# Optimization experiments

Hardware: AMD Instinct MI355X
Metric: run time of the kernel (lower is better)

The kernel has to match this reference:

```python
import jax, jax.numpy as jnp
import numpy as np

IN_SIZE = 512
HID = 512
BATCH = 65536


def setup_inputs() -> dict:
    key = jax.random.key(0)
    ks = jax.random.split(key, 20)
    s = 1.0 / np.sqrt(IN_SIZE)
    sh = 1.0 / np.sqrt(HID)
    d = {
        "inputs": jax.random.normal(ks[0], (BATCH, IN_SIZE), jnp.float32),
        "state": jax.random.normal(ks[1], (BATCH, HID), jnp.float32),
        "parent_state": jax.random.normal(ks[2], (BATCH, HID), jnp.float32),
    }
    # input-path linears (with bias), torch Linear layout: W [out, in], y = x @ W.T + b
    for i, name in enumerate(["w_a", "w_r", "w_r1", "w_c"]):
        d[name + "_w"] = jax.random.uniform(ks[3 + 2 * i], (HID, IN_SIZE), jnp.float32, -s, s)
        d[name + "_b"] = jax.random.uniform(ks[4 + 2 * i], (HID,), jnp.float32, -s, s)
    # state-path and parent-path linears (no bias)
    for i, name in enumerate(["u_a", "u_r", "u_r1", "u_c", "p_a", "p_r", "p_r1", "p_c"]):
        d[name + "_w"] = jax.random.uniform(ks[11 + i], (HID, HID), jnp.float32, -sh, sh)
    return d


def reference(inputs, state, parent_state,
              w_a_w, w_a_b, w_r_w, w_r_b, w_r1_w, w_r1_b, w_c_w, w_c_b,
              u_a_w, u_r_w, u_r1_w, u_c_w,
              p_a_w, p_r_w, p_r1_w, p_c_w):
    def lin(x, w, b=None):
        y = x @ w.T
        return y if b is None else y + b

    att = jax.nn.sigmoid(lin(inputs, w_a_w, w_a_b) + lin(state, u_a_w) + lin(parent_state, p_a_w))
    r = jax.nn.sigmoid(lin(inputs, w_r_w, w_r_b) + lin(state, u_r_w) + lin(parent_state, p_r_w))
    r1 = jax.nn.sigmoid(lin(inputs, w_r1_w, w_r1_b) + lin(state, u_r1_w) + lin(parent_state, p_r1_w))
    c = jnp.tanh(lin(inputs, w_c_w, w_c_b) + lin(state * r, u_c_w) + lin(parent_state * r1, p_c_w))
    new_h = att * c + (1.0 - att) * state
    return new_h
```

## Files before the change

### kernel.cpp

```cpp
#include <hip/hip_runtime.h>
#include <stdint.h>


typedef unsigned short u16;
using bf16x8 = __attribute__((ext_vector_type(8))) __bf16;
using f32x4  = __attribute__((ext_vector_type(4))) float;

__device__ __forceinline__ u16 f2bf(float f) {
    __bf16 b = (__bf16)f;
    union { __bf16 b; u16 u; } v; v.b = b;
    return v.u;
}
__device__ __forceinline__ uint32_t f2bf2(float lo, float hi) {
    return (uint32_t)f2bf(lo) | ((uint32_t)f2bf(hi) << 16);
}
__device__ __forceinline__ float bf2f(u16 s) {
    union { uint32_t u; float f; } v; v.u = ((uint32_t)s) << 16;
    return v.f;
}
__device__ __forceinline__ void load_lds16(const void* g, void* l) {
    __builtin_amdgcn_global_load_lds(
        (const __attribute__((address_space(1))) uint32_t*)g,
        (__attribute__((address_space(3))) uint32_t*)l, 16, 0, 0);
}
__device__ __forceinline__ void fence_bar() {
    asm volatile("" ::: "memory");
    __builtin_amdgcn_s_barrier();
    asm volatile("" ::: "memory");
}

__global__ void prep_weights(
    const float* __restrict__ wa, const float* __restrict__ ua, const float* __restrict__ pa,
    const float* __restrict__ wrg, const float* __restrict__ ur, const float* __restrict__ pr,
    const float* __restrict__ wr1, const float* __restrict__ ur1, const float* __restrict__ pr1,
    const float* __restrict__ wcc, const float* __restrict__ uc, const float* __restrict__ pc,
    u16* __restrict__ B1, u16* __restrict__ B2)
{
    int idx = blockIdx.x * 256 + threadIdx.x;
    const int T1 = 1536 * 1536;
    if (idx < T1) {
        int n = idx / 1536, k = idx - n * 1536;
        int g = n >> 9, nn = n & 511;
        int o = k >> 9, kk = k & 511;
        const float* s;
        if (g == 0)      s = (o == 0) ? wa  : (o == 1) ? ua  : pa;
        else if (g == 1) s = (o == 0) ? wrg : (o == 1) ? ur  : pr;
        else             s = (o == 0) ? wr1 : (o == 1) ? ur1 : pr1;
        B1[idx] = f2bf(s[nn * 512 + kk]);
    } else {
        int j = idx - T1;
        if (j < 512 * 1536) {
            int n = j / 1536, k = j - n * 1536;
            int o = k >> 9, kk = k & 511;
            const float* s = (o == 0) ? wcc : (o == 1) ? uc : pc;
            B2[j] = f2bf(s[n * 512 + kk]);
        }
    }
}

__global__ void cast_inputs(const float* __restrict__ X, const float* __restrict__ H,
                            const float* __restrict__ P,
                            u16* __restrict__ Xb, u16* __restrict__ Hb, u16* __restrict__ Pb)
{
    const long long MAT8 = (65536LL * 512) / 8;
    for (long long t = (long long)blockIdx.x * 256 + threadIdx.x;
         t < 3 * MAT8; t += (long long)gridDim.x * 256) {
        int m = (int)(t >> 22);
        long long e = (t & (MAT8 - 1)) * 8;
        const float* s = (m == 0) ? X : (m == 1) ? H : P;
        u16* d = (m == 0) ? Xb : (m == 1) ? Hb : Pb;
        f32x4 a = *(const f32x4*)(s + e);
        f32x4 b = *(const f32x4*)(s + e + 4);
        uint4 q;
        q.x = f2bf2(a.x, a.y); q.y = f2bf2(a.z, a.w);
        q.z = f2bf2(b.x, b.y); q.w = f2bf2(b.z, b.w);
        *(uint4*)(d + e) = q;
    }
}

template<int MODE>
__global__ __launch_bounds__(512, 2)
void gemm256(const u16* __restrict__ A0, const u16* __restrict__ A1s, const u16* __restrict__ A2s,
             const u16* __restrict__ Bw,
             const float* __restrict__ bias0, const float* __restrict__ bias1,
             const float* __restrict__ bias2,
             const u16* __restrict__ HbP, const u16* __restrict__ PbP,
             const float* __restrict__ Hf,
             float* __restrict__ outp, u16* __restrict__ hrw, u16* __restrict__ pr1w)
{
    __shared__ u16 lds[65536];
    constexpr int NT = 24;

    const int tid  = threadIdx.x;
    const int lane = tid & 63;
    const int wv   = tid >> 6;
    const int wr   = wv >> 2;
    const int wc   = wv & 3;

    int panel, ntl;
    const int xcd = blockIdx.x & 7;
    const int idx = blockIdx.x >> 3;
    if (MODE == 1) { panel = xcd * 32 + idx / 6;    ntl = idx % 6; }
    else           { panel = xcd * 32 + (idx >> 1); ntl = idx & 1; }
    const int m0 = panel * 256;
    const int n0 = ntl * 256;

    const int srow = tid >> 3;
    const int scg  = ((tid & 7) ^ (srow & 7)) * 8;
    const int ldst = srow * 64 + (tid & 7) * 8;

    const int ofsA = srow * 512 + scg;
    const int ofsB = srow * 1536 + scg;
    const u16* const bA0 = A0  + (size_t)m0 * 512;
    const u16* const bA1 = A1s + (size_t)m0 * 512;
    const u16* const bA2 = A2s + (size_t)m0 * 512;
    const u16* const bB  = Bw  + (size_t)n0 * 1536;
    u16* const ldA = lds + ldst;
    u16* const ldB = lds + 16384 + ldst;

    const int fr = lane & 15;
    const int fk = (lane >> 4) * 8;
    const int sw = (lane & 7) * 8;
    const int c0 = fk ^ sw;
    const int c1 = (32 + fk) ^ sw;
    const int aOff = (wr * 128 + fr) * 64;
    const int bOff = 16384 + (wc * 64 + fr) * 64;

    f32x4 acc[8][4];
    const f32x4 vzero = {0.0f, 0.0f, 0.0f, 0.0f};
#pragma unroll
    for (int i = 0; i < 8; ++i)
#pragma unroll
        for (int j = 0; j < 4; ++j) acc[i][j] = vzero;

    auto stA = [&](const u16* sA, int buf, int h) {
        const u16* g = sA + ofsA + h * 65536;
        u16* l = ldA + buf * 32768 + h * 8192;
        load_lds16(g, l);
        load_lds16(g + 64 * 512, l + 4096);
    };
    auto stB = [&](int T, int h) {
        const u16* g = bB + T * 64 + ofsB + h * 196608;
        u16* l = ldB + (T & 1) * 32768 + h * 8192;
        load_lds16(g, l);
        load_lds16(g + 64 * 1536, l + 4096);
    };

    stA(bA0, 0, 0); stA(bA0, 0, 1);
    stB(0, 0); stB(0, 1);
    stB(1, 0); stB(1, 1);
    asm volatile("s_waitcnt vmcnt(4)" ::: "memory");
    fence_bar();

    for (int T = 0; T < NT; ++T) {
        const int cb = (T & 1) * 32768;
        const int Tn = T + 1;
        const u16* sAn = ((Tn < 8) ? bA0 : (Tn < 16) ? bA1 : bA2) + (Tn & 7) * 64;
        const u16* const pa0 = lds + (cb + aOff + c0);
        const u16* const pa1 = lds + (cb + aOff + c1);
        const u16* const pb0 = lds + (cb + bOff + c0);
        const u16* const pb1 = lds + (cb + bOff + c1);

        bf16x8 bF[4][2];
#pragma unroll
        for (int q = 0; q < 4; ++q) {
            if (q == 0) {
#pragma unroll
                for (int j = 0; j < 4; ++j) {
                    bF[j][0] = *(const bf16x8*)(pb0 + j * 1024);
                    bF[j][1] = *(const bf16x8*)(pb1 + j * 1024);
                }
            }
            bf16x8 aF[2][2];
#pragma unroll
            for (int i = 0; i < 2; ++i) {
                aF[i][0] = *(const bf16x8*)(pa0 + (q * 2 + i) * 1024);
                aF[i][1] = *(const bf16x8*)(pa1 + (q * 2 + i) * 1024);
            }

            if (q == 0) { if (T < NT - 1) stA(sAn, Tn & 1, 0); }
            if (q == 1) { if (T < NT - 1) stA(sAn, Tn & 1, 1);
                          if (T < NT - 2) stB(T + 2, 0); }
            if (q == 2) { if (T < NT - 2) stB(T + 2, 1); }

            fence_bar();
            asm volatile("s_waitcnt lgkmcnt(0)" ::: "memory");
            __builtin_amdgcn_sched_barrier(0);
            __builtin_amdgcn_s_setprio(1);
#pragma unroll
            for (int i = 0; i < 2; ++i)
#pragma unroll
                for (int j = 0; j < 4; ++j)
#pragma unroll
                    for (int ks = 0; ks < 2; ++ks)
                        acc[q * 2 + i][j] = __builtin_amdgcn_mfma_f32_16x16x32_bf16(
                            aF[i][ks], bF[j][ks], acc[q * 2 + i][j], 0, 0, 0);
            __builtin_amdgcn_s_setprio(0);
            if (q == 3) {
                if (T < NT - 2)       asm volatile("s_waitcnt vmcnt(4)" ::: "memory");
                else if (T == NT - 2) asm volatile("s_waitcnt vmcnt(0)" ::: "memory");
            }
            fence_bar();
        }
    }

    const int rbase = m0 + wr * 128 + (lane >> 4) * 4;
    if (MODE == 1) {
        const int g = ntl >> 1;
        const float* bias = (g == 0) ? bias0 : (g == 1) ? bias1 : bias2;
        const int ncb = (ntl & 1) * 256 + wc * 64;
#pragma unroll
        for (int i = 0; i < 8; ++i)
#pragma unroll
            for (int j = 0; j < 4; ++j) {
                const int nn = ncb + j * 16 + fr;
                const float b = bias[nn];
                int off = (rbase + i * 16) * 512 + nn;
#pragma unroll
                for (int jj = 0; jj < 4; ++jj, off += 512) {
                    float v = acc[i][j][jj] + b;
                    float s = 1.0f / (1.0f + __expf(-v));
                    if (g == 0)      outp[off] = s;
                    else if (g == 1) hrw[off]  = f2bf(s * bf2f(HbP[off]));
                    else             pr1w[off] = f2bf(s * bf2f(PbP[off]));
                }
            }
    } else {
        const int ncb = n0 + wc * 64;
#pragma unroll
        for (int i = 0; i < 8; ++i)
#pragma unroll
            for (int j = 0; j < 4; ++j) {
                const int nn = ncb + j * 16 + fr;
                const float b = bias0[nn];
                int off = (rbase + i * 16) * 512 + nn;
#pragma unroll
                for (int jj = 0; jj < 4; ++jj, off += 512) {
                    float v = acc[i][j][jj] + b;
                    float e = __expf(2.0f * v);
                    float ct = 1.0f - 2.0f / (e + 1.0f);
                    float a = outp[off];
                    outp[off] = a * ct + (1.0f - a) * Hf[off];
                }
            }
    }
}

__global__ __launch_bounds__(256, 2)
void k1_small(const float* __restrict__ X, const float* __restrict__ H,
              const float* __restrict__ P, const u16* __restrict__ B1,
              const float* __restrict__ ba, const float* __restrict__ br,
              const float* __restrict__ br1,
              float* __restrict__ attf, u16* __restrict__ hrw, u16* __restrict__ pr1w)
{
    __shared__ u16 Ab[2][128 * 64];
    __shared__ u16 Bb[2][128 * 64];
    const int tid = threadIdx.x, lane = tid & 63, w = tid >> 6;
    const int wr = w >> 1, wc = w & 1;
    const int bid = blockIdx.x, xcd = bid & 7, idx = bid >> 3;
    const int panel = idx / 12, ntl = idx - panel * 12;
    const int m0 = (xcd * 64 + panel) * 128, n0 = ntl * 128;
    const int srow = w * 32 + (lane >> 3);
    const int scol = ((lane & 7) ^ (lane >> 3)) * 8;
    const int arow = tid >> 4, acol = (tid & 15) * 4;
    const int aswz = acol ^ ((arow & 7) << 3);
    f32x4 acc[4][4];
    const f32x4 vz = {0, 0, 0, 0};
#pragma unroll
    for (int i = 0; i < 4; ++i)
#pragma unroll
        for (int j = 0; j < 4; ++j) acc[i][j] = vz;
    f32x4 areg[8];
    auto issueA = [&](int kt) {
        const float* src = (kt < 8) ? X : (kt < 16) ? H : P;
        const float* base = src + (size_t)(m0 + arow) * 512 + (kt & 7) * 64 + acol;
#pragma unroll
        for (int rr = 0; rr < 8; ++rr)
            areg[rr] = *(const f32x4*)(base + (size_t)(rr * 16) * 512);
    };
    auto writeA = [&](int nb) {
#pragma unroll
        for (int rr = 0; rr < 8; ++rr) {
            uint2 q; q.x = f2bf2(areg[rr].x, areg[rr].y);
            q.y = f2bf2(areg[rr].z, areg[rr].w);
            *(uint2*)&Ab[nb][(arow + rr * 16) * 64 + aswz] = q;
        }
    };
    auto issueB = [&](int kt, int nb) {
        const u16* gb = B1 + (size_t)(n0 + srow) * 1536 + kt * 64 + scol;
        u16* lb = &Bb[nb][(w * 32) * 64];
#pragma unroll
        for (int c = 0; c < 4; ++c)
            load_lds16(gb + (size_t)c * 8 * 1536, lb + c * 8 * 64);
    };
    auto compute = [&](int cb) {
        const int rsw = (lane & 7) << 3, rb = lane & 15, hi8 = (lane >> 4) * 8;
#pragma unroll
        for (int ks = 0; ks < 2; ++ks) {
            bf16x8 af[4], bfr[4];
            const int col = (ks * 32 + hi8) ^ rsw;
#pragma unroll
            for (int fm = 0; fm < 4; ++fm)
                af[fm] = *(const bf16x8*)&Ab[cb][(wr * 64 + fm * 16 + rb) * 64 + col];
#pragma unroll
            for (int fn = 0; fn < 4; ++fn)
                bfr[fn] = *(const bf16x8*)&Bb[cb][(wc * 64 + fn * 16 + rb) * 64 + col];
#pragma unroll
            for (int fm = 0; fm < 4; ++fm)
#pragma unroll
                for (int fn = 0; fn < 4; ++fn)
                    acc[fm][fn] = __builtin_amdgcn_mfma_f32_16x16x32_bf16(
                        af[fm], bfr[fn], acc[fm][fn], 0, 0, 0);
        }
    };
    issueA(0); issueB(0, 0); writeA(0);
    __syncthreads();
    int cb = 0;
#pragma unroll 2
    for (int kt = 0; kt < 24; ++kt) {
        if (kt < 23) { issueA(kt + 1); issueB(kt + 1, cb ^ 1); }
        compute(cb);
        if (kt < 23) writeA(cb ^ 1);
        __syncthreads();
        cb ^= 1;
    }
    const int gate = ntl >> 2;
    const float* bias = (gate == 0) ? ba : (gate == 1) ? br : br1;
    const int nnb = (ntl & 3) * 128 + wc * 64;
    const int rl = (lane >> 4) * 4, cl = lane & 15;
#pragma unroll
    for (int fm = 0; fm < 4; ++fm)
#pragma unroll
        for (int fn = 0; fn < 4; ++fn) {
            const int nn = nnb + fn * 16 + cl;
            const float b = bias[nn];
#pragma unroll
            for (int j = 0; j < 4; ++j) {
                const int row = m0 + wr * 64 + fm * 16 + rl + j;
                const size_t off = (size_t)row * 512 + nn;
                float v = acc[fm][fn][j] + b;
                float s = 1.0f / (1.0f + __expf(-v));
                if (gate == 0)      attf[off] = s;
                else if (gate == 1) hrw[off]  = f2bf(s * H[off]);
                else                pr1w[off] = f2bf(s * P[off]);
            }
        }
}

__global__ __launch_bounds__(256, 2)
void k2_small(const float* __restrict__ X, const float* __restrict__ H,
              const u16* __restrict__ B2, const float* __restrict__ bc,
              const u16* __restrict__ hrw, const u16* __restrict__ pr1w,
              float* outp)
{
    __shared__ u16 Ab[2][128 * 64];
    __shared__ u16 Bb[2][128 * 64];
    const int tid = threadIdx.x, lane = tid & 63, w = tid >> 6;
    const int wr = w >> 1, wc = w & 1;
    const int bid = blockIdx.x, xcd = bid & 7, idx = bid >> 3;
    const int panel = idx >> 2, ntl = idx & 3;
    const int m0 = (xcd * 64 + panel) * 128, n0 = ntl * 128;
    const int srow = w * 32 + (lane >> 3);
    const int scol = ((lane & 7) ^ (lane >> 3)) * 8;
    const int arow = tid >> 4, acol = (tid & 15) * 4;
    const int aswz = acol ^ ((arow & 7) << 3);
    f32x4 acc[4][4];
    const f32x4 vz = {0, 0, 0, 0};
#pragma unroll
    for (int i = 0; i < 4; ++i)
#pragma unroll
        for (int j = 0; j < 4; ++j) acc[i][j] = vz;
    f32x4 areg[8];
    auto issueA = [&](int kt, int nb) {
        if (kt >= 8) {
            const u16* src = (kt < 16) ? hrw : pr1w;
            const u16* gb = src + (size_t)(m0 + srow) * 512 + (kt & 7) * 64 + scol;
            u16* lb = &Ab[nb][(w * 32) * 64];
#pragma unroll
            for (int c = 0; c < 4; ++c)
                load_lds16(gb + (size_t)c * 8 * 512, lb + c * 8 * 64);
        } else {
            const float* base = X + (size_t)(m0 + arow) * 512 + (kt & 7) * 64 + acol;
#pragma unroll
            for (int rr = 0; rr < 8; ++rr)
                areg[rr] = *(const f32x4*)(base + (size_t)(rr * 16) * 512);
        }
    };
    auto writeA = [&](int kt, int nb) {
        if (kt < 8) {
#pragma unroll
            for (int rr = 0; rr < 8; ++rr) {
                uint2 q; q.x = f2bf2(areg[rr].x, areg[rr].y);
                q.y = f2bf2(areg[rr].z, areg[rr].w);
                *(uint2*)&Ab[nb][(arow + rr * 16) * 64 + aswz] = q;
            }
        }
    };
    auto issueB = [&](int kt, int nb) {
        const u16* gb = B2 + (size_t)(n0 + srow) * 1536 + kt * 64 + scol;
        u16* lb = &Bb[nb][(w * 32) * 64];
#pragma unroll
        for (int c = 0; c < 4; ++c)
            load_lds16(gb + (size_t)c * 8 * 1536, lb + c * 8 * 64);
    };
    auto compute = [&](int cb) {
        const int rsw = (lane & 7) << 3, rb = lane & 15, hi8 = (lane >> 4) * 8;
#pragma unroll
        for (int ks = 0; ks < 2; ++ks) {
            bf16x8 af[4], bfr[4];
            const int col = (ks * 32 + hi8) ^ rsw;
#pragma unroll
            for (int fm = 0; fm < 4; ++fm)
                af[fm] = *(const bf16x8*)&Ab[cb][(wr * 64 + fm * 16 + rb) * 64 + col];
#pragma unroll
            for (int fn = 0; fn < 4; ++fn)
                bfr[fn] = *(const bf16x8*)&Bb[cb][(wc * 64 + fn * 16 + rb) * 64 + col];
#pragma unroll
            for (int fm = 0; fm < 4; ++fm)
#pragma unroll
                for (int fn = 0; fn < 4; ++fn)
                    acc[fm][fn] = __builtin_amdgcn_mfma_f32_16x16x32_bf16(
                        af[fm], bfr[fn], acc[fm][fn], 0, 0, 0);
        }
    };
    issueA(0, 0); issueB(0, 0); writeA(0, 0);
    __syncthreads();
    int cb = 0;
#pragma unroll 2
    for (int kt = 0; kt < 24; ++kt) {
        if (kt < 23) { issueA(kt + 1, cb ^ 1); issueB(kt + 1, cb ^ 1); }
        compute(cb);
        if (kt < 23) writeA(kt + 1, cb ^ 1);
        __syncthreads();
        cb ^= 1;
    }
    const int nnb = n0 + wc * 64;
    const int rl = (lane >> 4) * 4, cl = lane & 15;
#pragma unroll
    for (int fm = 0; fm < 4; ++fm)
#pragma unroll
        for (int fn = 0; fn < 4; ++fn) {
            const int nn = nnb + fn * 16 + cl;
            const float b = bc[nn];
#pragma unroll
            for (int j = 0; j < 4; ++j) {
                const int row = m0 + wr * 64 + fm * 16 + rl + j;
                const size_t off = (size_t)row * 512 + nn;
                float v = acc[fm][fn][j] + b;
                float e = __expf(2.0f * v);
                float ct = 1.0f - 2.0f / (e + 1.0f);
                float a = outp[off];
                outp[off] = a * ct + (1.0f - a) * H[off];
            }
        }
}

extern "C" void kernel_launch(void* const* d_in, const int* in_sizes, int n_in,
                              void* d_out, int out_size, void* d_ws, size_t ws_size,
                              hipStream_t stream)
{
    const float* X   = (const float*)d_in[0];
    const float* H   = (const float*)d_in[1];
    const float* P   = (const float*)d_in[2];
    const float* wa  = (const float*)d_in[3];
    const float* ba  = (const float*)d_in[4];
    const float* wrg = (const float*)d_in[5];
    const float* br  = (const float*)d_in[6];
    const float* wr1 = (const float*)d_in[7];
    const float* br1 = (const float*)d_in[8];
    const float* wcc = (const float*)d_in[9];
    const float* bc  = (const float*)d_in[10];
    const float* ua  = (const float*)d_in[11];
    const float* ur  = (const float*)d_in[12];
    const float* ur1 = (const float*)d_in[13];
    const float* uc  = (const float*)d_in[14];
    const float* pa  = (const float*)d_in[15];
    const float* pr  = (const float*)d_in[16];
    const float* pr1 = (const float*)d_in[17];
    const float* pc  = (const float*)d_in[18];

    char* ws = (char*)d_ws;
    u16* B1   = (u16*)(ws);
    u16* B2   = (u16*)(ws + (size_t)4718592);
    u16* hrp  = (u16*)(ws + (size_t)6291456);
    u16* pr1p = (u16*)(ws + (size_t)73400320);
    u16* Xb   = (u16*)(ws + (size_t)140509184);
    u16* Hb   = (u16*)(ws + (size_t)207618048);
    u16* Pb   = (u16*)(ws + (size_t)274726912);
    float* out = (float*)d_out;

    const bool big = ws_size >= (size_t)341835776ULL;

    prep_weights<<<12288, 256, 0, stream>>>(wa, ua, pa, wrg, ur, pr, wr1, ur1, pr1,
                                            wcc, uc, pc, B1, B2);
    if (big) {
        cast_inputs<<<3072, 256, 0, stream>>>(X, H, P, Xb, Hb, Pb);
        gemm256<1><<<1536, 512, 0, stream>>>(Xb, Hb, Pb, B1, ba, br, br1,
                                             Hb, Pb, nullptr, out, hrp, pr1p);
        gemm256<2><<<512, 512, 0, stream>>>(Xb, hrp, pr1p, B2, bc, nullptr, nullptr,
                                            nullptr, nullptr, H, out, nullptr, nullptr);
    } else {
        k1_small<<<6144, 256, 0, stream>>>(X, H, P, B1, ba, br, br1, out, hrp, pr1p);
        k2_small<<<2048, 256, 0, stream>>>(X, H, B2, bc, hrp, pr1p, out);
    }
}
```

Before: 750.6 us.

## Restructure GEMM main loop to two-phase compute with prefetch after barrier

Result: slower. 799.0 us (+6.5%).

```diff
diff --git a/kernel.cpp b/kernel.cpp
--- a/kernel.cpp
+++ b/kernel.cpp
@@ -133,29 +133,31 @@
 #pragma unroll
         for (int j = 0; j < 4; ++j) acc[i][j] = vzero;
 
-    auto stA = [&](const u16* sA, int buf, int h) {
-        const u16* g = sA + ofsA + h * 65536;
-        u16* l = ldA + buf * 32768 + h * 8192;
-        load_lds16(g, l);
-        load_lds16(g + 64 * 512, l + 4096);
-    };
-    auto stB = [&](int T, int h) {
-        const u16* g = bB + T * 64 + ofsB + h * 196608;
-        u16* l = ldB + (T & 1) * 32768 + h * 8192;
-        load_lds16(g, l);
-        load_lds16(g + 64 * 1536, l + 4096);
-    };
-
-    stA(bA0, 0, 0); stA(bA0, 0, 1);
-    stB(0, 0); stB(0, 1);
-    stB(1, 0); stB(1, 1);
-    asm volatile("s_waitcnt vmcnt(4)" ::: "memory");
+    auto stA = [&](int T) {
+        const u16* src = (T < 8) ? bA0 : (T < 16) ? bA1 : bA2;
+        const u16* g = src + (T & 7) * 64 + ofsA;
+        u16* l = ldA + (T & 1) * 32768;
+        load_lds16(g,             l);
+        load_lds16(g +  64 * 512, l + 4096);
+        load_lds16(g + 128 * 512, l + 8192);
+        load_lds16(g + 192 * 512, l + 12288);
+    };
+    auto stB = [&](int T) {
+        const u16* g = bB + T * 64 + ofsB;
+        u16* l = ldB + (T & 1) * 32768;
+        load_lds16(g,              l);
+        load_lds16(g +  64 * 1536, l + 4096);
+        load_lds16(g + 128 * 1536, l + 8192);
+        load_lds16(g + 192 * 1536, l + 12288);
+    };
+
+    stA(0); stB(0);
+    stA(1); stB(1);
+    asm volatile("s_waitcnt vmcnt(8)" ::: "memory");
     fence_bar();
 
     for (int T = 0; T < NT; ++T) {
         const int cb = (T & 1) * 32768;
-        const int Tn = T + 1;
-        const u16* sAn = ((Tn < 8) ? bA0 : (Tn < 16) ? bA1 : bA2) + (Tn & 7) * 64;
         const u16* const pa0 = lds + (cb + aOff + c0);
         const u16* const pa1 = lds + (cb + aOff + c1);
         const u16* const pb0 = lds + (cb + bOff + c0);
@@ -163,45 +165,51 @@
 
         bf16x8 bF[4][2];
 #pragma unroll
-        for (int q = 0; q < 4; ++q) {
-            if (q == 0) {
-#pragma unroll
-                for (int j = 0; j < 4; ++j) {
-                    bF[j][0] = *(const bf16x8*)(pb0 + j * 1024);
-                    bF[j][1] = *(const bf16x8*)(pb1 + j * 1024);
-                }
-            }
-            bf16x8 aF[2][2];
-#pragma unroll
-            for (int i = 0; i < 2; ++i) {
-                aF[i][0] = *(const bf16x8*)(pa0 + (q * 2 + i) * 1024);
-                aF[i][1] = *(const bf16x8*)(pa1 + (q * 2 + i) * 1024);
-            }
-
-            if (q == 0) { if (T < NT - 1) stA(sAn, Tn & 1, 0); }
-            if (q == 1) { if (T < NT - 1) stA(sAn, Tn & 1, 1);
-                          if (T < NT - 2) stB(T + 2, 0); }
-            if (q == 2) { if (T < NT - 2) stB(T + 2, 1); }
-
-            fence_bar();
-            asm volatile("s_waitcnt lgkmcnt(0)" ::: "memory");
-            __builtin_amdgcn_sched_barrier(0);
-            __builtin_amdgcn_s_setprio(1);
-#pragma unroll
-            for (int i = 0; i < 2; ++i)
-#pragma unroll
-                for (int j = 0; j < 4; ++j)
-#pragma unroll
-                    for (int ks = 0; ks < 2; ++ks)
-                        acc[q * 2 + i][j] = __builtin_amdgcn_mfma_f32_16x16x32_bf16(
-                            aF[i][ks], bF[j][ks], acc[q * 2 + i][j], 0, 0, 0);
-            __builtin_amdgcn_s_setprio(0);
-            if (q == 3) {
-                if (T < NT - 2)       asm volatile("s_waitcnt vmcnt(4)" ::: "memory");
-                else if (T == NT - 2) asm volatile("s_waitcnt vmcnt(0)" ::: "memory");
-            }
-            fence_bar();
-        }
+        for (int j = 0; j < 4; ++j) {
+            bF[j][0] = *(const bf16x8*)(pb0 + j * 1024);
+            bF[j][1] = *(const bf16x8*)(pb1 + j * 1024);
+        }
+        bf16x8 aF0[4][2];
+#pragma unroll
+        for (int m = 0; m < 4; ++m) {
+            aF0[m][0] = *(const bf16x8*)(pa0 + m * 1024);
+            aF0[m][1] = *(const bf16x8*)(pa1 + m * 1024);
+        }
+        __builtin_amdgcn_s_setprio(1);
+#pragma unroll
+        for (int m = 0; m < 4; ++m)
+#pragma unroll
+            for (int j = 0; j < 4; ++j)
+#pragma unroll
+                for (int ks = 0; ks < 2; ++ks)
+                    acc[m][j] = __builtin_amdgcn_mfma_f32_16x16x32_bf16(
+                        aF0[m][ks], bF[j][ks], acc[m][j], 0, 0, 0);
+        __builtin_amdgcn_s_setprio(0);
+        bf16x8 aF1[4][2];
+#pragma unroll
+        for (int m = 0; m < 4; ++m) {
+            aF1[m][0] = *(const bf16x8*)(pa0 + (4 + m) * 1024);
+            aF1[m][1] = *(const bf16x8*)(pa1 + (4 + m) * 1024);
+        }
+        __builtin_amdgcn_s_setprio(1);
+#pragma unroll
+        for (int m = 0; m < 4; ++m)
+#pragma unroll
+            for (int j = 0; j < 4; ++j)
+#pragma unroll
+                for (int ks = 0; ks < 2; ++ks)
+                    acc[4 + m][j] = __builtin_amdgcn_mfma_f32_16x16x32_bf16(
+                        aF1[m][ks], bF[j][ks], acc[4 + m][j], 0, 0, 0);
+        __builtin_amdgcn_s_setprio(0);
+
+        fence_bar();
+        if (T < NT - 2) {
+            stA(T + 2); stB(T + 2);
+            asm volatile("s_waitcnt vmcnt(8)" ::: "memory");
+        } else if (T == NT - 2) {
+            asm volatile("s_waitcnt vmcnt(0)" ::: "memory");
+        }
+        fence_bar();
     }
 
     const int rbase = m0 + wr * 128 + (lane >> 4) * 4;
```
